# Kernel optimization log

Measured on AMD Instinct MI355X. Metric: run time of the kernel, lower is better.

## Reference

```python
import jax, jax.numpy as jnp
import numpy as np

B, N1, N2 = 4, 16384, 4096   # scenes, fine points/scene, coarse points/scene
CIN, COUT = 512, 256
K = 3
EPS_BN = 1e-5
EPS_D = 1e-8


def setup_inputs() -> dict:
    key = jax.random.key(0)
    ks = jax.random.split(key, 6)
    return {
        "point_1": jax.random.uniform(ks[0], (B * N1, 3), dtype=jnp.float32),
        "feat_1": jax.random.normal(ks[1], (B * N1, COUT), dtype=jnp.float32) * 0.1,
        "point_2": jax.random.uniform(ks[2], (B * N2, 3), dtype=jnp.float32),
        "feat_2": jax.random.normal(ks[3], (B * N2, CIN), dtype=jnp.float32) * 0.1,
        "W1": jax.random.normal(ks[4], (COUT, COUT), dtype=jnp.float32) / np.sqrt(COUT).astype(np.float32),
        "b1": jnp.zeros((COUT,), jnp.float32),
        "g1": jnp.ones((COUT,), jnp.float32),
        "beta1": jnp.zeros((COUT,), jnp.float32),
        "W2": jax.random.normal(ks[5], (CIN, COUT), dtype=jnp.float32) / np.sqrt(CIN).astype(np.float32),
        "b2": jnp.zeros((COUT,), jnp.float32),
        "g2": jnp.ones((COUT,), jnp.float32),
        "beta2": jnp.zeros((COUT,), jnp.float32),
        # equal-sized segments: row_splits = [0, N, 2N, ...]
        "row_splits_1": jnp.arange(B + 1, dtype=jnp.int32) * N1,
        "row_splits_2": jnp.arange(B + 1, dtype=jnp.int32) * N2,
    }


def _bn(x, gamma, beta):
    # BatchNorm1d, training mode (biased variance, as in torch)
    mu = x.mean(0)
    var = x.var(0)
    return gamma * (x - mu) * jax.lax.rsqrt(var + EPS_BN) + beta


def reference(point_1, feat_1, point_2, feat_2,
              W1, b1, g1, beta1, W2, b2, g2, beta2,
              row_splits_1, row_splits_2):
    # linear1(feat_1): Linear + BN + ReLU
    f1 = jax.nn.relu(_bn(feat_1 @ W1 + b1, g1, beta1))          # [B*N1, COUT]
    # linear2(feat_2): Linear + BN + ReLU
    f2 = jax.nn.relu(_bn(feat_2 @ W2 + b2, g2, beta2))          # [B*N2, COUT]

    # batched KNN (equal row_splits -> reshape into [B, n, 3])
    q = point_1.reshape(B, N1, 3)
    p = point_2.reshape(B, N2, 3)
    d2 = ((q * q).sum(-1)[:, :, None]
          + (p * p).sum(-1)[:, None, :]
          - 2.0 * jnp.einsum("bnd,bmd->bnm", q, p))             # [B, N1, N2] squared dists
    neg_d, idx = jax.lax.top_k(-d2, K)                           # [B, N1, K]
    dist = jnp.maximum(-neg_d, 0.0)

    # inverse-distance weights (knn search is non-differentiable in the original)
    recip = 1.0 / (dist + EPS_D)
    w = jax.lax.stop_gradient(recip / recip.sum(-1, keepdims=True))  # [B, N1, K]

    # gather + weighted sum (three-interpolate)
    f2b = f2.reshape(B, N2, COUT)
    gathered = f2b[jnp.arange(B)[:, None, None], idx]            # [B, N1, K, COUT]
    interp = (gathered * w[..., None]).sum(2).reshape(B * N1, COUT)

    return f1 + interp
```

## Files before the change

### kernel.cpp

```cpp
#include <hip/hip_runtime.h>
#include <hip/hip_bf16.h>
#include <math.h>

#define N1R 65536
#define N2R 16384
#define NPB 4096
#define NQB 16384
#define CC  256
#define ASTRIDE 40
#define NCELL 512
#define GRID_FAIL_R2 0.015625f

typedef __attribute__((ext_vector_type(4))) float v4f;
typedef __attribute__((ext_vector_type(8))) short v8s;

static __device__ __forceinline__ short f2bs(float f) {
    union { __hip_bfloat16 h; short s; } u;
    u.h = __float2bfloat16(f);
    return u.s;
}

static __device__ __forceinline__ int cell_of(float x, float y, float z) {
    const int cx = min(7, (int)(x * 8.0f));
    const int cy = min(7, (int)(y * 8.0f));
    const int cz = min(7, (int)(z * 8.0f));
    return (cz << 6) | (cy << 3) | cx;
}

static __device__ __forceinline__ void ins3(float d, int si,
    float& b0, float& b1, float& b2, int& i0, int& i1, int& i2)
{
    const bool lt0 = (d < b0) | ((d == b0) & (si < i0));
    const bool lt1 = (d < b1) | ((d == b1) & (si < i1));
    const bool lt2 = (d < b2) | ((d == b2) & (si < i2));
    b2 = lt1 ? b1 : (lt2 ? d : b2);   i2 = lt1 ? i1 : (lt2 ? si : i2);
    b1 = lt0 ? b0 : (lt1 ? d : b1);   i1 = lt0 ? i0 : (lt1 ? si : i1);
    b0 = lt0 ? d  : b0;               i0 = lt0 ? si : i0;
}

__global__ __launch_bounds__(256)
void prep_kernel(const float* __restrict__ W1f, const float* __restrict__ W2f,
                 short* __restrict__ WT1, short* __restrict__ WT2,
                 const float* __restrict__ p2, const float* __restrict__ p1,
                 float4* __restrict__ paug,
                 int* __restrict__ counts_p, int* __restrict__ counts_q)
{
#pragma clang fp contract(off)
    const int bid = blockIdx.x;
    if (bid < 768) {
        const int i = bid * 256 + threadIdx.x;
        if (i < 65536) {
            const int k = i >> 8, n = i & 255;
            WT1[(size_t)n * 256 + k] = f2bs(W1f[i]);
        } else {
            const int j = i - 65536;
            const int k = j >> 8, n = j & 255;
            WT2[(size_t)n * 512 + k] = f2bs(W2f[j]);
        }
    } else if (bid < 832) {
        const int i = (bid - 768) * 256 + threadIdx.x;
        const float x = p2[(size_t)i * 3 + 0];
        const float y = p2[(size_t)i * 3 + 1];
        const float z = p2[(size_t)i * 3 + 2];
        float4 v;
        v.x = x; v.y = y; v.z = z;
        v.w = (x * x + y * y) + z * z;
        paug[i] = v;
        const int b = i >> 12;
        atomicAdd(&counts_p[b * NCELL + cell_of(x, y, z)], 1);
    } else {
        const int i = (bid - 832) * 256 + threadIdx.x;
        const float x = p1[(size_t)i * 3 + 0];
        const float y = p1[(size_t)i * 3 + 1];
        const float z = p1[(size_t)i * 3 + 2];
        const int b = i >> 14;
        atomicAdd(&counts_q[b * NCELL + cell_of(x, y, z)], 1);
    }
}

__global__ __launch_bounds__(512)
void prefix_kernel(const int* __restrict__ counts_p, int* __restrict__ cursors_p,
                   int* __restrict__ starts_p,
                   const int* __restrict__ counts_q, int* __restrict__ cursors_q)
{
    __shared__ int sw[8];
    __shared__ int sbase[8];
    const int t = threadIdx.x;
    const int lane = t & 63, wid = t >> 6;
    for (int a = 0; a < 8; ++a) {
        const int b = a & 3;
        const int* cnt = (a < 4) ? counts_p + b * NCELL : counts_q + b * NCELL;
        const int v = cnt[t];
        int incl = v;
#pragma unroll
        for (int off = 1; off < 64; off <<= 1) {
            const int u = __shfl_up(incl, off);
            incl += (lane >= off) ? u : 0;
        }
        if (lane == 63) sw[wid] = incl;
        __syncthreads();
        if (t == 0) {
            int s = 0;
#pragma unroll
            for (int w = 0; w < 8; ++w) { const int x = sw[w]; sbase[w] = s; s += x; }
        }
        __syncthreads();
        const int inclT = incl + sbase[wid];
        const int excl = inclT - v;
        if (a < 4) {
            starts_p[b * 513 + t] = excl;
            if (t == 511) starts_p[b * 513 + 512] = inclT;
            cursors_p[b * NCELL + t] = excl;
        } else {
            cursors_q[b * NCELL + t] = excl;
        }
        __syncthreads();
    }
}

__global__ __launch_bounds__(256)
void scatter_kernel(const float4* __restrict__ paug, const float* __restrict__ p1,
                    int* __restrict__ cursors_p, int* __restrict__ cursors_q,
                    float4* __restrict__ sortedP, unsigned short* __restrict__ sIdx,
                    unsigned short* __restrict__ qlist)
{
    if (blockIdx.x < 64) {
        const int i = blockIdx.x * 256 + threadIdx.x;
        const float4 v = paug[i];
        const int b = i >> 12;
        const int cell = cell_of(v.x, v.y, v.z);
        const int pos = atomicAdd(&cursors_p[b * NCELL + cell], 1);
        sortedP[(size_t)b * NPB + pos] = v;
        sIdx[(size_t)b * NPB + pos] = (unsigned short)(i & 4095);
    } else {
        const int i = (blockIdx.x - 64) * 256 + threadIdx.x;
        const float x = p1[(size_t)i * 3 + 0];
        const float y = p1[(size_t)i * 3 + 1];
        const float z = p1[(size_t)i * 3 + 2];
        const int b = i >> 14;
        const int cell = cell_of(x, y, z);
        const int pos = atomicAdd(&cursors_q[b * NCELL + cell], 1);
        qlist[(size_t)b * NQB + pos] = (unsigned short)(i & 16383);
    }
}

template<int BM>
static __device__ __forceinline__ void gemm_body(
    int bx, int by,
    const float* __restrict__ X, const short* __restrict__ WT,
    const float* __restrict__ bias, float* __restrict__ Y,
    float* __restrict__ partS, float* __restrict__ partQ,
    int Kdim, short* __restrict__ As0, short* __restrict__ As1)
{
    constexpr int MI  = BM / 32;
    constexpr int NPF = BM / 32;
    constexpr int TPR = 256 / BM;
    constexpr int FPT = BM / 8;

    const int bm0 = bx * BM;
    const int bn0 = by * 128;
    const int wave = threadIdx.x >> 6;
    const int lane = threadIdx.x & 63;
    const int wm0 = (wave >> 1) * (BM / 2);
    const int wn0 = (wave & 1) * 64;
    const int col = lane & 15, quad = lane >> 4;

    const int srow = threadIdx.x / TPR;
    const int skh  = (threadIdx.x % TPR) * FPT;
    const float* sbase = X + (size_t)(bm0 + srow) * Kdim + skh;
    short* sdst0 = As0 + srow * ASTRIDE + skh;
    short* sdst1 = As1 + srow * ASTRIDE + skh;

    v4f acc[MI][4];
#pragma unroll
    for (int i = 0; i < MI; ++i)
#pragma unroll
        for (int j = 0; j < 4; ++j) acc[i][j] = (v4f){0.f, 0.f, 0.f, 0.f};

    const short* wbase = WT + (size_t)(bn0 + wn0 + col) * Kdim + quad * 8;

    v4f pf[NPF];
#pragma unroll
    for (int i = 0; i < NPF; ++i) pf[i] = *(const v4f*)(sbase + i * 4);
    {
        v8s wv;
#pragma unroll
        for (int j = 0; j < NPF / 2; ++j) {
#pragma unroll
            for (int t = 0; t < 4; ++t) {
                wv[t]     = f2bs(pf[2 * j][t]);
                wv[t + 4] = f2bs(pf[2 * j + 1][t]);
            }
            *(v8s*)(sdst0 + j * 8) = wv;
        }
    }
    if (32 < Kdim)
#pragma unroll
        for (int i = 0; i < NPF; ++i) pf[i] = *(const v4f*)(sbase + 32 + i * 4);

    const int NC = Kdim >> 5;
    for (int c = 0; c < NC; ++c) {
        const int k0 = c << 5;
        const bool more = (c + 1 < NC);

        v8s wv[NPF / 2];
        if (more) {
#pragma unroll
            for (int j = 0; j < NPF / 2; ++j)
#pragma unroll
                for (int t = 0; t < 4; ++t) {
                    wv[j][t]     = f2bs(pf[2 * j][t]);
                    wv[j][t + 4] = f2bs(pf[2 * j + 1][t]);
                }
        }
        __syncthreads();
        if (more) {
            short* sd = (c & 1) ? sdst0 : sdst1;
#pragma unroll
            for (int j = 0; j < NPF / 2; ++j) *(v8s*)(sd + j * 8) = wv[j];
        }

        v8s bf[4];
#pragma unroll
        for (int ni = 0; ni < 4; ++ni)
            bf[ni] = *(const v8s*)(wbase + (size_t)(ni * 16) * Kdim + k0);

        if (c + 2 < NC) {
            const float* np = sbase + k0 + 64;
#pragma unroll
            for (int i = 0; i < NPF; ++i) pf[i] = *(const v4f*)(np + i * 4);
        }

        const short* bufc = (c & 1) ? As1 : As0;
        v8s a[MI];
#pragma unroll
        for (int mi = 0; mi < MI; ++mi)
            a[mi] = *(const v8s*)(bufc + (wm0 + mi * 16 + col) * ASTRIDE + quad * 8);
#pragma unroll
        for (int mi = 0; mi < MI; ++mi)
#pragma unroll
            for (int ni = 0; ni < 4; ++ni)
                acc[mi][ni] = __builtin_amdgcn_mfma_f32_16x16x32_bf16(a[mi], bf[ni], acc[mi][ni], 0, 0, 0);
    }

    float* pS = partS + (size_t)(bx * 2 + (wave >> 1)) * CC;
    float* pQ = partQ + (size_t)(bx * 2 + (wave >> 1)) * CC;
#pragma unroll
    for (int ni = 0; ni < 4; ++ni) {
        const int n = bn0 + wn0 + ni * 16 + col;
        const float bv = bias[n];
        float s = 0.f, q = 0.f;
#pragma unroll
        for (int mi = 0; mi < MI; ++mi) {
            const int m = bm0 + wm0 + mi * 16 + quad * 4;
#pragma unroll
            for (int r = 0; r < 4; ++r) {
                const float y = acc[mi][ni][r] + bv;
                Y[(size_t)(m + r) * CC + n] = y;
                s += y; q += y * y;
            }
        }
        s += __shfl_xor(s, 16); q += __shfl_xor(q, 16);
        s += __shfl_xor(s, 32); q += __shfl_xor(q, 32);
        if (quad == 0) { pS[n] = s; pQ[n] = q; }
    }
}

__global__ __launch_bounds__(256)
void gemm_both_kernel(const float* __restrict__ feat1, const short* __restrict__ WT1,
                      const float* __restrict__ b1, float* __restrict__ Y1,
                      float* __restrict__ pS1, float* __restrict__ pQ1,
                      const float* __restrict__ feat2, const short* __restrict__ WT2,
                      const float* __restrict__ b2, float* __restrict__ Y2,
                      float* __restrict__ pS2, float* __restrict__ pQ2)
{
    __shared__ short As[2][128 * ASTRIDE];
    const int id = blockIdx.x;
    if (id < 1024) {
        gemm_body<128>(id >> 1, id & 1, feat1, WT1, b1, Y1, pS1, pQ1, 256,
                       As[0], As[1]);
    } else {
        const int j = id - 1024;
        gemm_body<64>(j >> 1, j & 1, feat2, WT2, b2, Y2, pS2, pQ2, 512,
                      As[0], As[1]);
    }
}

__global__ __launch_bounds__(256)
void stat_reduce_kernel(const float* __restrict__ pS1, const float* __restrict__ pQ1,
                        const float* __restrict__ pS2, const float* __restrict__ pQ2,
                        float* __restrict__ stats)
{
    const int c = threadIdx.x;
    const bool two = blockIdx.x >= 16;
    const float* pS = two ? pS2 : pS1;
    const float* pQ = two ? pQ2 : pQ1;
    const int r0 = (two ? (blockIdx.x - 16) : blockIdx.x) * 64;
    float s = 0.f, q = 0.f;
    for (int r = r0; r < r0 + 64; ++r) {
        s += pS[(size_t)r * CC + c];
        q += pQ[(size_t)r * CC + c];
    }
    float* st = stats + (two ? 512 : 0);
    atomicAdd(&st[c], s);
    atomicAdd(&st[256 + c], q);
}

__global__ __launch_bounds__(512)
void finalize_kernel(const float* __restrict__ sums,
                     const float* __restrict__ g1, const float* __restrict__ be1,
                     const float* __restrict__ g2, const float* __restrict__ be2,
                     float* __restrict__ ac)
{
    const int t = threadIdx.x;
    const int c = t & 255;
    const int which = t >> 8;
    const float* s = sums + which * 512;
    const double n = which ? (double)N2R : (double)N1R;
    const double mu = (double)s[c] / n;
    const double var = (double)s[c + 256] / n - mu * mu;
    const float g  = which ? g2[c]  : g1[c];
    const float be = which ? be2[c] : be1[c];
    const double a  = (double)g / sqrt(var + 1e-5);
    const double cv = (double)be - a * mu;
    ac[which * 512 + c]       = (float)a;
    ac[which * 512 + 256 + c] = (float)cv;
}

__global__ __launch_bounds__(256)
void knn_grid_kernel(const float* __restrict__ p1,
                     const float4* __restrict__ sortedP,
                     const unsigned short* __restrict__ sIdx16,
                     const int* __restrict__ starts_p,
                     const unsigned short* __restrict__ qlist,
                     int* __restrict__ idx_out, float* __restrict__ w_out,
                     int* __restrict__ failCount, int* __restrict__ failList)
{
#pragma clang fp contract(off)
    __shared__ float4 sP[NPB];
    __shared__ unsigned short sI[NPB];
    __shared__ int sS[513];
    __shared__ float mD[128 * 3];
    __shared__ int   mI[128 * 3];

    const int b = blockIdx.x >> 7;
    const int slot0 = (blockIdx.x & 127) * 128;
    const int tid = threadIdx.x;
    const int lq = tid & 127;
    const int half = tid >> 7;

    {
        const float4* gp = sortedP + (size_t)b * NPB;
        for (int i = tid; i < NPB; i += 256) sP[i] = gp[i];
        const unsigned int* gi = (const unsigned int*)(sIdx16 + (size_t)b * NPB);
        unsigned int* li = (unsigned int*)sI;
        for (int i = tid; i < NPB / 2; i += 256) li[i] = gi[i];
        const int* gs = starts_p + b * 513;
        for (int i = tid; i < 513; i += 256) sS[i] = gs[i];
    }

    const int q = qlist[(size_t)b * NQB + slot0 + lq];
    const int qid = b * NQB + q;
    const float qx = p1[(size_t)qid * 3 + 0];
    const float qy = p1[(size_t)qid * 3 + 1];
    const float qz = p1[(size_t)qid * 3 + 2];
    const float qq = (qx * qx + qy * qy) + qz * qz;
    const int cqx = min(7, (int)(qx * 8.0f));
    const int cqy = min(7, (int)(qy * 8.0f));
    const int cqz = min(7, (int)(qz * 8.0f));

    __syncthreads();

    float b0 = 3.0e38f, b1 = 3.0e38f, b2 = 3.0e38f;
    int i0 = 0x7fffffff, i1 = 0x7fffffff, i2 = 0x7fffffff;

    int n = 0;
    for (int dz = -1; dz <= 1; ++dz)
        for (int dy = -1; dy <= 1; ++dy)
            for (int dx = -1; dx <= 1; ++dx, ++n) {
                if (half ? (n < 14) : (n >= 14)) continue;
                const int cz = cqz + dz, cy = cqy + dy, cx = cqx + dx;
                if (((unsigned)cz | (unsigned)cy | (unsigned)cx) > 7u) continue;
                const int cell = (cz << 6) | (cy << 3) | cx;
                const int ks = sS[cell], ke = sS[cell + 1];
                for (int k = ks; k < ke; ++k) {
                    const float4 P = sP[k];
                    const int si = sI[k];
                    const float dot = fmaf(qz, P.z, fmaf(qy, P.y, qx * P.x));
                    const float d = fmaf(-2.0f, dot, qq + P.w);
                    ins3(d, si, b0, b1, b2, i0, i1, i2);
                }
            }

    if (half) {
        mD[lq * 3 + 0] = b0; mD[lq * 3 + 1] = b1; mD[lq * 3 + 2] = b2;
        mI[lq * 3 + 0] = i0; mI[lq * 3 + 1] = i1; mI[lq * 3 + 2] = i2;
    }
    __syncthreads();
    if (!half) {
#pragma unroll
        for (int r = 0; r < 3; ++r)
            ins3(mD[lq * 3 + r], mI[lq * 3 + r], b0, b1, b2, i0, i1, i2);

        if (!(b2 < GRID_FAIL_R2)) {
            const int p = atomicAdd(failCount, 1);
            if (p < N1R) failList[p] = qid;
        }
        const float r0 = 1.0f / (fmaxf(b0, 0.0f) + 1e-8f);
        const float r1 = 1.0f / (fmaxf(b1, 0.0f) + 1e-8f);
        const float r2 = 1.0f / (fmaxf(b2, 0.0f) + 1e-8f);
        const float rs = (r0 + r1) + r2;
        idx_out[(size_t)qid * 3 + 0] = i0;
        idx_out[(size_t)qid * 3 + 1] = i1;
        idx_out[(size_t)qid * 3 + 2] = i2;
        w_out[(size_t)qid * 3 + 0] = r0 / rs;
        w_out[(size_t)qid * 3 + 1] = r1 / rs;
        w_out[(size_t)qid * 3 + 2] = r2 / rs;
    }
}

__global__ __launch_bounds__(256)
void knn_bf_kernel(const float* __restrict__ p1,
                   const float4* __restrict__ paug,
                   const int* __restrict__ failCount,
                   const int* __restrict__ failList,
                   int* __restrict__ idx_out, float* __restrict__ w_out)
{
#pragma clang fp contract(off)
    const int nf = min(*failCount, N1R);
    const int gw = (blockIdx.x * 256 + threadIdx.x) >> 6;
    const int lane = threadIdx.x & 63;
    const int nw = (gridDim.x * 256) >> 6;

    for (int fi = gw; fi < nf; fi += nw) {
        const int qid = failList[fi];
        const int b = qid >> 14;
        const float qx = p1[(size_t)qid * 3 + 0];
        const float qy = p1[(size_t)qid * 3 + 1];
        const float qz = p1[(size_t)qid * 3 + 2];
        const float qq = (qx * qx + qy * qy) + qz * qz;

        float b0 = 3.0e38f, b1 = 3.0e38f, b2 = 3.0e38f;
        int i0 = 0x7fffffff, i1 = 0x7fffffff, i2 = 0x7fffffff;

        const float4* pb = paug + (size_t)b * NPB;
        for (int j = lane; j < NPB; j += 64) {
            const float4 P = pb[j];
            const float dot = fmaf(qz, P.z, fmaf(qy, P.y, qx * P.x));
            const float d = fmaf(-2.0f, dot, qq + P.w);
            ins3(d, j, b0, b1, b2, i0, i1, i2);
        }
        for (int m = 1; m < 64; m <<= 1) {
            const float c0 = __shfl_xor(b0, m), c1 = __shfl_xor(b1, m), c2 = __shfl_xor(b2, m);
            const int j0 = __shfl_xor(i0, m), j1 = __shfl_xor(i1, m), j2 = __shfl_xor(i2, m);
            ins3(c0, j0, b0, b1, b2, i0, i1, i2);
            ins3(c1, j1, b0, b1, b2, i0, i1, i2);
            ins3(c2, j2, b0, b1, b2, i0, i1, i2);
        }
        if (lane == 0) {
            const float r0 = 1.0f / (fmaxf(b0, 0.0f) + 1e-8f);
            const float r1 = 1.0f / (fmaxf(b1, 0.0f) + 1e-8f);
            const float r2 = 1.0f / (fmaxf(b2, 0.0f) + 1e-8f);
            const float rs = (r0 + r1) + r2;
            idx_out[(size_t)qid * 3 + 0] = i0;
            idx_out[(size_t)qid * 3 + 1] = i1;
            idx_out[(size_t)qid * 3 + 2] = i2;
            w_out[(size_t)qid * 3 + 0] = r0 / rs;
            w_out[(size_t)qid * 3 + 1] = r1 / rs;
            w_out[(size_t)qid * 3 + 2] = r2 / rs;
        }
    }
}

__global__ __launch_bounds__(256)
void final_kernel(float* __restrict__ Y1out,
                  const float* __restrict__ Y2raw,
                  const float* __restrict__ ac,
                  const int* __restrict__ idx, const float* __restrict__ w,
                  const unsigned short* __restrict__ qlist)
{
    const int slot = blockIdx.x * 4 + (threadIdx.x >> 6);
    const int b = slot >> 14;
    const int r = b * NQB + qlist[slot];
    const int cg = threadIdx.x & 63;

    v4f a1 = *(const v4f*)(ac + cg * 4);
    v4f c1 = *(const v4f*)(ac + 256 + cg * 4);
    v4f a2 = *(const v4f*)(ac + 512 + cg * 4);
    v4f c2 = *(const v4f*)(ac + 768 + cg * 4);
    v4f y = *(const v4f*)(Y1out + (size_t)r * CC + cg * 4);
    v4f s;
#pragma unroll
    for (int j = 0; j < 4; ++j)
        s[j] = fmaxf(fmaf(a1[j], y[j], c1[j]), 0.f);

    const int*   ir = idx + (size_t)r * 3;
    const float* wr = w   + (size_t)r * 3;
#pragma unroll
    for (int k = 0; k < 3; ++k) {
        const int id = ir[k];
        const float wk = wr[k];
        v4f g = *(const v4f*)(Y2raw + ((size_t)(b * NPB + id)) * CC + cg * 4);
#pragma unroll
        for (int j = 0; j < 4; ++j) {
            const float gv = fmaxf(fmaf(a2[j], g[j], c2[j]), 0.f);
            s[j] = fmaf(wk, gv, s[j]);
        }
    }
    *(v4f*)(Y1out + (size_t)r * CC + cg * 4) = s;
}

extern "C" void kernel_launch(void* const* d_in, const int* in_sizes, int n_in,
                              void* d_out, int out_size, void* d_ws, size_t ws_size,
                              hipStream_t stream)
{
    const float* point1 = (const float*)d_in[0];
    const float* feat1  = (const float*)d_in[1];
    const float* point2 = (const float*)d_in[2];
    const float* feat2  = (const float*)d_in[3];
    const float* W1     = (const float*)d_in[4];
    const float* b1     = (const float*)d_in[5];
    const float* g1     = (const float*)d_in[6];
    const float* beta1  = (const float*)d_in[7];
    const float* W2     = (const float*)d_in[8];
    const float* b2     = (const float*)d_in[9];
    const float* g2     = (const float*)d_in[10];
    const float* beta2  = (const float*)d_in[11];

    float* Y1 = (float*)d_out;

    char* ws = (char*)d_ws;
    float*          Y2       = (float*)ws;
    float*          stats    = (float*)(ws + (size_t)16777216);
    int*            counts_p = (int*)  (ws + (size_t)16781312);
    int*            counts_q = (int*)  (ws + (size_t)16789504);
    int*            failCnt  = (int*)  (ws + (size_t)16797696);
    int*            cursors_p= (int*)  (ws + (size_t)16801792);
    int*            cursors_q= (int*)  (ws + (size_t)16809984);
    int*            starts_p = (int*)  (ws + (size_t)16818176);
    float*          ac       = (float*)(ws + (size_t)16826624);
    unsigned short* sIdx16   = (unsigned short*)(ws + (size_t)16830720);
    unsigned short* qlist    = (unsigned short*)(ws + (size_t)16863488);
    int*            failList = (int*)  (ws + (size_t)16994560);
    float4*         sortedP  = (float4*)(ws + (size_t)17256704);
    int*            idxb     = (int*)  (ws + (size_t)17518848);
    float*          wb       = (float*)(ws + (size_t)18305280);
    short*          WT1      = (short*)(ws + (size_t)19091712);
    short*          WT2      = (short*)(ws + (size_t)19222784);
    float4*         paug     = (float4*)(ws + (size_t)19484928);
    float*          partS1   = (float*)(ws + (size_t)19747072);
    float*          partQ1   = (float*)(ws + (size_t)20795648);
    float*          partS2   = (float*)(ws + (size_t)21844224);
    float*          partQ2   = (float*)(ws + (size_t)22368512);

    hipMemsetAsync(stats, 0, 24576, stream);

    prep_kernel<<<1088, 256, 0, stream>>>(W1, W2, WT1, WT2, point2, point1,
                                          paug, counts_p, counts_q);
    prefix_kernel<<<1, 512, 0, stream>>>(counts_p, cursors_p, starts_p, counts_q, cursors_q);
    scatter_kernel<<<320, 256, 0, stream>>>(paug, point1, cursors_p, cursors_q,
                                            sortedP, sIdx16, qlist);

    gemm_both_kernel<<<1536, 256, 0, stream>>>(feat1, WT1, b1, Y1, partS1, partQ1,
                                               feat2, WT2, b2, Y2, partS2, partQ2);

    stat_reduce_kernel<<<24, 256, 0, stream>>>(partS1, partQ1, partS2, partQ2, stats);
    finalize_kernel<<<1, 512, 0, stream>>>(stats, g1, beta1, g2, beta2, ac);

    knn_grid_kernel<<<512, 256, 0, stream>>>(point1, sortedP, sIdx16, starts_p,
                                             qlist, idxb, wb, failCnt, failList);
    knn_bf_kernel<<<256, 256, 0, stream>>>(point1, paug, failCnt, failList, idxb, wb);

    final_kernel<<<N1R / 4, 256, 0, stream>>>(Y1, Y2, ac, idxb, wb, qlist);
}
```

Baseline: 306.0 us.

## Fold brute-force KNN fallback into final kernel and shrink feat1 GEMM tiles

Removes the separate brute-force KNN kernel and its atomic fail list. Queries that fail the grid search are now marked with a negative index and recomputed inline by the wave inside the final interpolation kernel. Separately, the feat1 GEMM moves from 128-row to 64-row tiles, doubling its block count, and the partial-statistics buffers and reduce grid are resized to match. This removes one launch and the global atomic, at the cost of wave divergence in the final kernel when failures occur and more partial-stat traffic.

```diff
diff --git a/kernel.cpp b/kernel.cpp
--- a/kernel.cpp
+++ b/kernel.cpp
@@ -274,13 +274,13 @@
                       const float* __restrict__ b2, float* __restrict__ Y2,
                       float* __restrict__ pS2, float* __restrict__ pQ2)
 {
-    __shared__ short As[2][128 * ASTRIDE];
+    __shared__ short As[2][64 * ASTRIDE];
     const int id = blockIdx.x;
-    if (id < 1024) {
-        gemm_body<128>(id >> 1, id & 1, feat1, WT1, b1, Y1, pS1, pQ1, 256,
-                       As[0], As[1]);
+    if (id < 2048) {
+        gemm_body<64>(id >> 1, id & 1, feat1, WT1, b1, Y1, pS1, pQ1, 256,
+                      As[0], As[1]);
     } else {
-        const int j = id - 1024;
+        const int j = id - 2048;
         gemm_body<64>(j >> 1, j & 1, feat2, WT2, b2, Y2, pS2, pQ2, 512,
                       As[0], As[1]);
     }
@@ -292,10 +292,10 @@
                         float* __restrict__ stats)
 {
     const int c = threadIdx.x;
-    const bool two = blockIdx.x >= 16;
+    const bool two = blockIdx.x >= 32;
     const float* pS = two ? pS2 : pS1;
     const float* pQ = two ? pQ2 : pQ1;
-    const int r0 = (two ? (blockIdx.x - 16) : blockIdx.x) * 64;
+    const int r0 = (two ? (blockIdx.x - 32) : blockIdx.x) * 64;
     float s = 0.f, q = 0.f;
     for (int r = r0; r < r0 + 64; ++r) {
         s += pS[(size_t)r * CC + c];
@@ -333,8 +333,7 @@
                      const unsigned short* __restrict__ sIdx16,
                      const int* __restrict__ starts_p,
                      const unsigned short* __restrict__ qlist,
-                     int* __restrict__ idx_out, float* __restrict__ w_out,
-                     int* __restrict__ failCount, int* __restrict__ failList)
+                     int* __restrict__ idx_out, float* __restrict__ w_out)
 {
 #pragma clang fp contract(off)
     __shared__ float4 sP[NPB];
@@ -402,10 +401,8 @@
         for (int r = 0; r < 3; ++r)
             ins3(mD[lq * 3 + r], mI[lq * 3 + r], b0, b1, b2, i0, i1, i2);
 
-        if (!(b2 < GRID_FAIL_R2)) {
-            const int p = atomicAdd(failCount, 1);
-            if (p < N1R) failList[p] = qid;
-        }
+        if (!(b2 < GRID_FAIL_R2)) i0 = -1;
+
         const float r0 = 1.0f / (fmaxf(b0, 0.0f) + 1e-8f);
         const float r1 = 1.0f / (fmaxf(b1, 0.0f) + 1e-8f);
         const float r2 = 1.0f / (fmaxf(b2, 0.0f) + 1e-8f);
@@ -420,31 +417,34 @@
 }
 
 __global__ __launch_bounds__(256)
-void knn_bf_kernel(const float* __restrict__ p1,
-                   const float4* __restrict__ paug,
-                   const int* __restrict__ failCount,
-                   const int* __restrict__ failList,
-                   int* __restrict__ idx_out, float* __restrict__ w_out)
+void final_kernel(float* __restrict__ Y1out,
+                  const float* __restrict__ Y2raw,
+                  const float* __restrict__ ac,
+                  const int* __restrict__ idx, const float* __restrict__ w,
+                  const unsigned short* __restrict__ qlist,
+                  const float* __restrict__ p1, const float4* __restrict__ paug)
 {
 #pragma clang fp contract(off)
-    const int nf = min(*failCount, N1R);
-    const int gw = (blockIdx.x * 256 + threadIdx.x) >> 6;
-    const int lane = threadIdx.x & 63;
-    const int nw = (gridDim.x * 256) >> 6;
-
-    for (int fi = gw; fi < nf; fi += nw) {
-        const int qid = failList[fi];
-        const int b = qid >> 14;
-        const float qx = p1[(size_t)qid * 3 + 0];
-        const float qy = p1[(size_t)qid * 3 + 1];
-        const float qz = p1[(size_t)qid * 3 + 2];
+    const int slot = blockIdx.x * 4 + (threadIdx.x >> 6);
+    const int b = slot >> 14;
+    const int r = b * NQB + qlist[slot];
+    const int cg = threadIdx.x & 63;
+
+    const int* ir = idx + (size_t)r * 3;
+    int i0 = ir[0], i1 = ir[1], i2 = ir[2];
+    float w0, w1, w2;
+    if (i0 >= 0) {
+        const float* wr = w + (size_t)r * 3;
+        w0 = wr[0]; w1 = wr[1]; w2 = wr[2];
+    } else {
+        const float qx = p1[(size_t)r * 3 + 0];
+        const float qy = p1[(size_t)r * 3 + 1];
+        const float qz = p1[(size_t)r * 3 + 2];
         const float qq = (qx * qx + qy * qy) + qz * qz;
-
         float b0 = 3.0e38f, b1 = 3.0e38f, b2 = 3.0e38f;
-        int i0 = 0x7fffffff, i1 = 0x7fffffff, i2 = 0x7fffffff;
-
+        i0 = 0x7fffffff; i1 = 0x7fffffff; i2 = 0x7fffffff;
         const float4* pb = paug + (size_t)b * NPB;
-        for (int j = lane; j < NPB; j += 64) {
+        for (int j = cg; j < NPB; j += 64) {
             const float4 P = pb[j];
             const float dot = fmaf(qz, P.z, fmaf(qy, P.y, qx * P.x));
             const float d = fmaf(-2.0f, dot, qq + P.w);
@@ -457,32 +457,12 @@
             ins3(c1, j1, b0, b1, b2, i0, i1, i2);
             ins3(c2, j2, b0, b1, b2, i0, i1, i2);
         }
-        if (lane == 0) {
-            const float r0 = 1.0f / (fmaxf(b0, 0.0f) + 1e-8f);
-            const float r1 = 1.0f / (fmaxf(b1, 0.0f) + 1e-8f);
-            const float r2 = 1.0f / (fmaxf(b2, 0.0f) + 1e-8f);
-            const float rs = (r0 + r1) + r2;
-            idx_out[(size_t)qid * 3 + 0] = i0;
-            idx_out[(size_t)qid * 3 + 1] = i1;
-            idx_out[(size_t)qid * 3 + 2] = i2;
-            w_out[(size_t)qid * 3 + 0] = r0 / rs;
-            w_out[(size_t)qid * 3 + 1] = r1 / rs;
-            w_out[(size_t)qid * 3 + 2] = r2 / rs;
-        }
-    }
-}
-
-__global__ __launch_bounds__(256)
-void final_kernel(float* __restrict__ Y1out,
-                  const float* __restrict__ Y2raw,
-                  const float* __restrict__ ac,
-                  const int* __restrict__ idx, const float* __restrict__ w,
-                  const unsigned short* __restrict__ qlist)
-{
-    const int slot = blockIdx.x * 4 + (threadIdx.x >> 6);
-    const int b = slot >> 14;
-    const int r = b * NQB + qlist[slot];
-    const int cg = threadIdx.x & 63;
+        const float r0 = 1.0f / (fmaxf(b0, 0.0f) + 1e-8f);
+        const float r1 = 1.0f / (fmaxf(b1, 0.0f) + 1e-8f);
+        const float r2 = 1.0f / (fmaxf(b2, 0.0f) + 1e-8f);
+        const float rs = (r0 + r1) + r2;
+        w0 = r0 / rs; w1 = r1 / rs; w2 = r2 / rs;
+    }
 
     v4f a1 = *(const v4f*)(ac + cg * 4);
     v4f c1 = *(const v4f*)(ac + 256 + cg * 4);
@@ -494,13 +474,12 @@
     for (int j = 0; j < 4; ++j)
         s[j] = fmaxf(fmaf(a1[j], y[j], c1[j]), 0.f);
 
-    const int*   ir = idx + (size_t)r * 3;
-    const float* wr = w   + (size_t)r * 3;
+    const int   id3[3] = { i0, i1, i2 };
+    const float wk3[3] = { w0, w1, w2 };
 #pragma unroll
     for (int k = 0; k < 3; ++k) {
-        const int id = ir[k];
-        const float wk = wr[k];
-        v4f g = *(const v4f*)(Y2raw + ((size_t)(b * NPB + id)) * CC + cg * 4);
+        const float wk = wk3[k];
+        v4f g = *(const v4f*)(Y2raw + ((size_t)(b * NPB + id3[k])) * CC + cg * 4);
 #pragma unroll
         for (int j = 0; j < 4; ++j) {
             const float gv = fmaxf(fmaf(a2[j], g[j], c2[j]), 0.f);
@@ -534,14 +513,12 @@
     float*          stats    = (float*)(ws + (size_t)16777216);
     int*            counts_p = (int*)  (ws + (size_t)16781312);
     int*            counts_q = (int*)  (ws + (size_t)16789504);
-    int*            failCnt  = (int*)  (ws + (size_t)16797696);
     int*            cursors_p= (int*)  (ws + (size_t)16801792);
     int*            cursors_q= (int*)  (ws + (size_t)16809984);
     int*            starts_p = (int*)  (ws + (size_t)16818176);
     float*          ac       = (float*)(ws + (size_t)16826624);
     unsigned short* sIdx16   = (unsigned short*)(ws + (size_t)16830720);
     unsigned short* qlist    = (unsigned short*)(ws + (size_t)16863488);
-    int*            failList = (int*)  (ws + (size_t)16994560);
     float4*         sortedP  = (float4*)(ws + (size_t)17256704);
     int*            idxb     = (int*)  (ws + (size_t)17518848);
     float*          wb       = (float*)(ws + (size_t)18305280);
@@ -549,9 +526,9 @@
     short*          WT2      = (short*)(ws + (size_t)19222784);
     float4*         paug     = (float4*)(ws + (size_t)19484928);
     float*          partS1   = (float*)(ws + (size_t)19747072);
-    float*          partQ1   = (float*)(ws + (size_t)20795648);
-    float*          partS2   = (float*)(ws + (size_t)21844224);
-    float*          partQ2   = (float*)(ws + (size_t)22368512);
+    float*          partQ1   = (float*)(ws + (size_t)21844224);
+    float*          partS2   = (float*)(ws + (size_t)23941376);
+    float*          partQ2   = (float*)(ws + (size_t)24465664);
 
     hipMemsetAsync(stats, 0, 24576, stream);
 
@@ -561,15 +538,15 @@
     scatter_kernel<<<320, 256, 0, stream>>>(paug, point1, cursors_p, cursors_q,
                                             sortedP, sIdx16, qlist);
 
-    gemm_both_kernel<<<1536, 256, 0, stream>>>(feat1, WT1, b1, Y1, partS1, partQ1,
+    gemm_both_kernel<<<2560, 256, 0, stream>>>(feat1, WT1, b1, Y1, partS1, partQ1,
                                                feat2, WT2, b2, Y2, partS2, partQ2);
 
-    stat_reduce_kernel<<<24, 256, 0, stream>>>(partS1, partQ1, partS2, partQ2, stats);
+    stat_reduce_kernel<<<40, 256, 0, stream>>>(partS1, partQ1, partS2, partQ2, stats);
     finalize_kernel<<<1, 512, 0, stream>>>(stats, g1, beta1, g2, beta2, ac);
 
     knn_grid_kernel<<<512, 256, 0, stream>>>(point1, sortedP, sIdx16, starts_p,
-                                             qlist, idxb, wb, failCnt, failList);
-    knn_bf_kernel<<<256, 256, 0, stream>>>(point1, paug, failCnt, failList, idxb, wb);
-
-    final_kernel<<<N1R / 4, 256, 0, stream>>>(Y1, Y2, ac, idxb, wb, qlist);
-}
+                                             qlist, idxb, wb);
+
+    final_kernel<<<N1R / 4, 256, 0, stream>>>(Y1, Y2, ac, idxb, wb, qlist,
+                                              point1, paug);
+}
```

Result: slower. 316.0 us (+3.3%).
